# Performance work log

Hardware: AMD Instinct MI355X
Metric: run time of the kernel (lower is better)

Reference implementation:

```python
import jax, jax.numpy as jnp
import numpy as np

N_NODES = 50000
N_EDGES = 600000
IN_FEATS = 128
HIDDEN = 256
OUT_FEATS = 64


def setup_inputs() -> dict:
    key = jax.random.key(0)
    ks = jax.random.split(key, 12)
    inv = lambda n: 1.0 / np.sqrt(n)
    return {
        "x": jax.random.normal(ks[0], (N_NODES, IN_FEATS), dtype=jnp.float32),
        "edge_index": jax.random.randint(ks[1], (2, N_EDGES), 0, N_NODES, dtype=jnp.int64),
        "W_sage": jax.random.normal(ks[2], (IN_FEATS, IN_FEATS), dtype=jnp.float32) * inv(IN_FEATS),
        "W1a": jax.random.normal(ks[3], (IN_FEATS, HIDDEN), dtype=jnp.float32) * inv(IN_FEATS),
        "b1a": jax.random.normal(ks[4], (HIDDEN,), dtype=jnp.float32) * 0.01,
        "W1b": jax.random.normal(ks[5], (HIDDEN, OUT_FEATS), dtype=jnp.float32) * inv(HIDDEN),
        "b1b": jax.random.normal(ks[6], (OUT_FEATS,), dtype=jnp.float32) * 0.01,
        "W2a": jax.random.normal(ks[7], (IN_FEATS, HIDDEN), dtype=jnp.float32) * inv(IN_FEATS),
        "b2a": jax.random.normal(ks[8], (HIDDEN,), dtype=jnp.float32) * 0.01,
        "W2b": jax.random.normal(ks[9], (HIDDEN, OUT_FEATS), dtype=jnp.float32) * inv(HIDDEN),
        "b2b": jax.random.normal(ks[10], (OUT_FEATS,), dtype=jnp.float32) * 0.01,
    }


def reference(x, edge_index, W_sage, W1a, b1a, W1b, b1b, W2a, b2a, W2b, b2b):
    n = x.shape[0]
    src, dst = edge_index[0], edge_index[1]
    # SAGEConv mean aggregation: mean over incoming neighbor (source) features at each target node
    summed = jax.ops.segment_sum(x[src], dst, num_segments=n)          # [N, in]
    deg = jax.ops.segment_sum(jnp.ones_like(src, dtype=x.dtype), dst, num_segments=n)
    mean = summed / jnp.maximum(deg, 1.0)[:, None]                     # nodes w/o neighbors -> 0
    x_1hop = mean @ W_sage                                             # lin_l, no root, no bias
    # dual MLP branches (dropout is identity in eval mode)
    out1 = jax.nn.relu(x @ W1a + b1a) @ W1b + b1b
    out2 = jax.nn.relu(x_1hop @ W2a + b2a) @ W2b + b2b
    return out1 + out2
```

## Files before the change

### kernel.cpp

```cpp
#include <hip/hip_runtime.h>

#define N_NODES 50000
#define N_PAD   50048
#define N_EDGES 600000
#define IN_F 128
#define HID 256
#define OUT_F 64
#define ROWS 16
#define SLOTS 56
#define NBLK (N_PAD / ROWS)

typedef __attribute__((ext_vector_type(8))) short bf16x8;
typedef __attribute__((ext_vector_type(4))) float f32x4;

__device__ inline short f2bf(float f) {
    unsigned u = __builtin_bit_cast(unsigned, f);
    u += 0x7fffu + ((u >> 16) & 1u);
    return (short)(u >> 16);
}
__device__ inline float bflo(unsigned u) { return __builtin_bit_cast(float, u << 16); }
__device__ inline float bfhi(unsigned u) { return __builtin_bit_cast(float, u & 0xffff0000u); }

__global__ __launch_bounds__(256) void k0_kernel(
    const float* __restrict__ Wsg, const float* __restrict__ W2a,
    float* __restrict__ Wc, int* __restrict__ cursor)
{
    const int bid = blockIdx.x, t = threadIdx.x;
    if (bid < 128) {
        float acc = 0.f;
        #pragma unroll 8
        for (int j = 0; j < 128; ++j)
            acc = fmaf(Wsg[bid * 128 + j], W2a[j * 256 + t], acc);
        Wc[bid * 256 + t] = acc;
    } else {
        int i = (bid - 128) * 256 + t;
        if (i < N_PAD) cursor[i] = 0;
    }
}

__global__ __launch_bounds__(256) void prep_build_kernel(
    const float* __restrict__ x, short* __restrict__ xb,
    const float* __restrict__ W1a, const float* __restrict__ W1b,
    const float* __restrict__ Wc,  const float* __restrict__ W2b,
    short* __restrict__ F1a, short* __restrict__ F1b,
    short* __restrict__ Fc,  short* __restrict__ F2b,
    const int* __restrict__ ei, int* __restrict__ cursor,
    unsigned short* __restrict__ esrc)
{
    const int bid = blockIdx.x, t = threadIdx.x;
    if (bid < 3125) {
        int i = bid * 256 + t;
        float4 a0 = *reinterpret_cast<const float4*>(x + (size_t)i * 8);
        float4 a1 = *reinterpret_cast<const float4*>(x + (size_t)i * 8 + 4);
        bf16x8 v;
        v[0] = f2bf(a0.x); v[1] = f2bf(a0.y); v[2] = f2bf(a0.z); v[3] = f2bf(a0.w);
        v[4] = f2bf(a1.x); v[5] = f2bf(a1.y); v[6] = f2bf(a1.z); v[7] = f2bf(a1.w);
        *reinterpret_cast<bf16x8*>(xb + (size_t)i * 8) = v;
    } else if (bid < 3173) {
        int cid = (bid - 3125) * 256 + t;
        const float* src; short* dst; int N, KST, base;
        if      (cid < 4096)  { src = W1a; dst = F1a; N = 256; KST = 4; base = 0; }
        else if (cid < 6144)  { src = W1b; dst = F1b; N = 64;  KST = 8; base = 4096; }
        else if (cid < 10240) { src = Wc;  dst = Fc;  N = 256; KST = 4; base = 6144; }
        else                  { src = W2b; dst = F2b; N = 64;  KST = 8; base = 10240; }
        int c = cid - base;
        int lane = c & 63;
        int rem = c >> 6;
        int ks = rem % KST;
        int nt = rem / KST;
        int col = nt * 16 + (lane & 15);
        int k0 = ks * 32 + (lane >> 4) * 8;
        bf16x8 v;
        #pragma unroll
        for (int j = 0; j < 8; ++j)
            v[j] = f2bf(src[(size_t)(k0 + j) * N + col]);
        *reinterpret_cast<bf16x8*>(dst + (size_t)c * 8) = v;
    } else {
        int e = (bid - 3173) * 256 + t;
        if (e < N_EDGES) {
            int src = ei[e];
            int dst = ei[N_EDGES + e];
            int p = atomicAdd(&cursor[dst], 1);
            if (p < SLOTS) esrc[(size_t)dst * SLOTS + p] = (unsigned short)src;
        }
    }
}

__device__ inline bf16x8 afrag_lds128(const short* S, int lane, int ks) {
    int row = lane & 15, g = lane >> 4;
    int chunk = (ks * 4 + g) ^ row;
    return *reinterpret_cast<const bf16x8*>(
        reinterpret_cast<const char*>(S) + row * 256 + chunk * 16);
}
__device__ inline bf16x8 afrag_lds256(const short* S, int lane, int ks) {
    int row = lane & 15, g = lane >> 4;
    int chunk = (ks * 4 + g) ^ row;
    return *reinterpret_cast<const bf16x8*>(
        reinterpret_cast<const char*>(S) + row * 512 + chunk * 16);
}

__device__ inline void stage1_relu(const bf16x8 afr[4], short* Hs,
                                   const short* __restrict__ Waf,
                                   const float* __restrict__ ba,
                                   int w, int lane)
{
    const int row16 = lane & 15, g = lane >> 4;
    #pragma unroll
    for (int i = 0; i < 4; ++i) {
        int nt = w * 4 + i;
        f32x4 acc = {0.f, 0.f, 0.f, 0.f};
        #pragma unroll
        for (int ks = 0; ks < 4; ++ks) {
            bf16x8 b = *reinterpret_cast<const bf16x8*>(
                Waf + ((size_t)(nt * 4 + ks) * 64 + lane) * 8);
            acc = __builtin_amdgcn_mfma_f32_16x16x32_bf16(afr[ks], b, acc, 0, 0, 0);
        }
        int col = nt * 16 + row16;
        float bias = ba[col];
        #pragma unroll
        for (int reg = 0; reg < 4; ++reg) {
            int hrow = g * 4 + reg;
            float v = fmaxf(acc[reg] + bias, 0.0f);
            *reinterpret_cast<short*>(reinterpret_cast<char*>(Hs)
                + hrow * 512 + ((((col >> 3) ^ hrow) & 31) * 16) + (col & 7) * 2) = f2bf(v);
        }
    }
}

__device__ inline f32x4 stage2_acc(const short* Hs, const short* __restrict__ Wbf,
                                   int w, int lane, f32x4 acc)
{
    #pragma unroll
    for (int ks = 0; ks < 8; ++ks) {
        bf16x8 a = afrag_lds256(Hs, lane, ks);
        bf16x8 b = *reinterpret_cast<const bf16x8*>(
            Wbf + ((size_t)(w * 8 + ks) * 64 + lane) * 8);
        acc = __builtin_amdgcn_mfma_f32_16x16x32_bf16(a, b, acc, 0, 0, 0);
    }
    return acc;
}

__global__ __launch_bounds__(256) void fused_kernel(
    const short* __restrict__ xb, const unsigned short* __restrict__ esrc,
    const int* __restrict__ deg,
    const short* __restrict__ F1a, const float* __restrict__ b1a,
    const short* __restrict__ F1b, const float* __restrict__ b1b,
    const short* __restrict__ Fc,  const float* __restrict__ b2a,
    const short* __restrict__ F2b, const float* __restrict__ b2b,
    float* __restrict__ out)
{
    __shared__ short Ms[16 * 128];
    __shared__ short Hs[16 * 256];
    const int t = threadIdx.x, w = t >> 6, lane = t & 63;
    const long r0 = (long)blockIdx.x * ROWS;
    const int row16 = lane & 15, g = lane >> 4;

    #pragma unroll
    for (int nn = 0; nn < 4; ++nn) {
        int row = w * 4 + nn;
        long node = r0 + row;
        int d = deg[node]; d = min(d, SLOTS);
        int slot = min(lane, SLOTS - 1);
        int my = esrc[(size_t)node * SLOTS + slot];
        float ax = 0.f, ay = 0.f;
        for (int j = 0; j < d; j += 16) {
            unsigned u[16];
            #pragma unroll
            for (int k = 0; k < 16; ++k) {
                int cidx = min(j + k, d - 1);
                int s = __builtin_amdgcn_readlane(my, cidx);
                u[k] = *reinterpret_cast<const unsigned*>(xb + (size_t)s * IN_F + lane * 2);
            }
            #pragma unroll
            for (int k = 0; k < 16; ++k) {
                float wk = (j + k < d) ? 1.0f : 0.0f;
                ax = fmaf(bflo(u[k]), wk, ax);
                ay = fmaf(bfhi(u[k]), wk, ay);
            }
        }
        float inv = (d > 0) ? 1.0f / (float)d : 0.0f;
        ax *= inv; ay *= inv;
        int chunk = (lane >> 2) ^ row;
        unsigned packed = (unsigned)(unsigned short)f2bf(ax)
                        | ((unsigned)(unsigned short)f2bf(ay) << 16);
        *reinterpret_cast<unsigned*>(reinterpret_cast<char*>(Ms)
            + row * 256 + chunk * 16 + (lane & 3) * 4) = packed;
    }
    __syncthreads();

    {
        bf16x8 afr[4];
        #pragma unroll
        for (int ks = 0; ks < 4; ++ks) afr[ks] = afrag_lds128(Ms, lane, ks);
        stage1_relu(afr, Hs, Fc, b2a, w, lane);
    }
    __syncthreads();

    f32x4 oacc = {0.f, 0.f, 0.f, 0.f};
    oacc = stage2_acc(Hs, F2b, w, lane, oacc);
    __syncthreads();

    {
        bf16x8 afr[4];
        const short* xrow = xb + (size_t)(r0 + row16) * IN_F + g * 8;
        #pragma unroll
        for (int ks = 0; ks < 4; ++ks)
            afr[ks] = *reinterpret_cast<const bf16x8*>(xrow + ks * 32);
        stage1_relu(afr, Hs, F1a, b1a, w, lane);
    }
    __syncthreads();

    oacc = stage2_acc(Hs, F1b, w, lane, oacc);
    {
        int col = w * 16 + row16;
        float bias = b1b[col] + b2b[col];
        #pragma unroll
        for (int reg = 0; reg < 4; ++reg) {
            long row = r0 + g * 4 + reg;
            if (row < N_NODES)
                out[row * OUT_F + col] = oacc[reg] + bias;
        }
    }
}

extern "C" void kernel_launch(void* const* d_in, const int* in_sizes, int n_in,
                              void* d_out, int out_size, void* d_ws, size_t ws_size,
                              hipStream_t stream)
{
    const float* x   = (const float*)d_in[0];
    const int*   ei  = (const int*)d_in[1];
    const float* Wsg = (const float*)d_in[2];
    const float* W1a = (const float*)d_in[3];
    const float* b1a = (const float*)d_in[4];
    const float* W1b = (const float*)d_in[5];
    const float* b1b = (const float*)d_in[6];
    const float* W2a = (const float*)d_in[7];
    const float* b2a = (const float*)d_in[8];
    const float* W2b = (const float*)d_in[9];
    const float* b2b = (const float*)d_in[10];
    float* out = (float*)d_out;

    int* cursor = (int*)d_ws;
    unsigned short* esrc = (unsigned short*)(cursor + N_PAD);
    float* Wc  = (float*)(esrc + (size_t)N_PAD * SLOTS);
    short* F1a = (short*)(Wc + 128 * 256);
    short* F1b = F1a + 4096 * 8;
    short* Fc  = F1b + 2048 * 8;
    short* F2b = Fc + 4096 * 8;
    short* xb  = F2b + 2048 * 8;

    k0_kernel<<<324, 256, 0, stream>>>(Wsg, W2a, Wc, cursor);
    prep_build_kernel<<<5517, 256, 0, stream>>>(x, xb, W1a, W1b, Wc, W2b,
                                                F1a, F1b, Fc, F2b,
                                                ei, cursor, esrc);
    fused_kernel<<<NBLK, 256, 0, stream>>>(xb, esrc, cursor,
                                           F1a, b1a, F1b, b1b,
                                           Fc, b2a, F2b, b2b, out);
}
```

Measured before the change: 119.6 us.

## Split edge bucketing into its own kernel and fuse weight combine into prep

Removes the separate k0 kernel. The Wsg·W2a product is now computed directly inside the prep kernel's Fc fragment packing, and the cursor is zeroed with hipMemsetAsync. Edge bucketing moves to a dedicated kernel that handles four edges per thread so the loads and atomics are batched. MFMA loops get s_setprio hints to favor matrix issue. Launch count stays the same; the fused Fc path does redundant FMAs per fragment, and the atomic kernel now runs alone instead of alongside the conversions.

```diff
diff --git a/kernel.cpp b/kernel.cpp
--- a/kernel.cpp
+++ b/kernel.cpp
@@ -9,6 +9,7 @@
 #define ROWS 16
 #define SLOTS 56
 #define NBLK (N_PAD / ROWS)
+#define EPT 4
 
 typedef __attribute__((ext_vector_type(8))) short bf16x8;
 typedef __attribute__((ext_vector_type(4))) float f32x4;
@@ -21,31 +22,37 @@
 __device__ inline float bflo(unsigned u) { return __builtin_bit_cast(float, u << 16); }
 __device__ inline float bfhi(unsigned u) { return __builtin_bit_cast(float, u & 0xffff0000u); }
 
-__global__ __launch_bounds__(256) void k0_kernel(
-    const float* __restrict__ Wsg, const float* __restrict__ W2a,
-    float* __restrict__ Wc, int* __restrict__ cursor)
-{
-    const int bid = blockIdx.x, t = threadIdx.x;
-    if (bid < 128) {
-        float acc = 0.f;
-        #pragma unroll 8
-        for (int j = 0; j < 128; ++j)
-            acc = fmaf(Wsg[bid * 128 + j], W2a[j * 256 + t], acc);
-        Wc[bid * 256 + t] = acc;
-    } else {
-        int i = (bid - 128) * 256 + t;
-        if (i < N_PAD) cursor[i] = 0;
-    }
-}
-
-__global__ __launch_bounds__(256) void prep_build_kernel(
-    const float* __restrict__ x, short* __restrict__ xb,
-    const float* __restrict__ W1a, const float* __restrict__ W1b,
-    const float* __restrict__ Wc,  const float* __restrict__ W2b,
-    short* __restrict__ F1a, short* __restrict__ F1b,
-    short* __restrict__ Fc,  short* __restrict__ F2b,
+__global__ __launch_bounds__(256) void build_kernel(
     const int* __restrict__ ei, int* __restrict__ cursor,
     unsigned short* __restrict__ esrc)
+{
+    int t0 = blockIdx.x * (256 * EPT) + threadIdx.x;
+    int src[EPT], dst[EPT], p[EPT];
+    bool v[EPT];
+    #pragma unroll
+    for (int i = 0; i < EPT; ++i) {
+        int e = t0 + i * 256;
+        v[i] = e < N_EDGES;
+        int ee = v[i] ? e : 0;
+        src[i] = ei[ee];
+        dst[i] = ei[N_EDGES + ee];
+    }
+    #pragma unroll
+    for (int i = 0; i < EPT; ++i)
+        p[i] = v[i] ? atomicAdd(&cursor[dst[i]], 1) : SLOTS;
+    #pragma unroll
+    for (int i = 0; i < EPT; ++i)
+        if (v[i] && p[i] < SLOTS)
+            esrc[(size_t)dst[i] * SLOTS + p[i]] = (unsigned short)src[i];
+}
+
+__global__ __launch_bounds__(256) void prep_kernel(
+    const float* __restrict__ x, short* __restrict__ xb,
+    const float* __restrict__ Wsg, const float* __restrict__ W2a,
+    const float* __restrict__ W1a, const float* __restrict__ W1b,
+    const float* __restrict__ W2b,
+    short* __restrict__ F1a, short* __restrict__ F1b,
+    short* __restrict__ Fc,  short* __restrict__ F2b)
 {
     const int bid = blockIdx.x, t = threadIdx.x;
     if (bid < 3125) {
@@ -56,12 +63,36 @@
         v[0] = f2bf(a0.x); v[1] = f2bf(a0.y); v[2] = f2bf(a0.z); v[3] = f2bf(a0.w);
         v[4] = f2bf(a1.x); v[5] = f2bf(a1.y); v[6] = f2bf(a1.z); v[7] = f2bf(a1.w);
         *reinterpret_cast<bf16x8*>(xb + (size_t)i * 8) = v;
-    } else if (bid < 3173) {
-        int cid = (bid - 3125) * 256 + t;
+        return;
+    }
+    int cid = (bid - 3125) * 256 + t;
+    if (cid >= 6144 && cid < 10240) {
+        int c = cid - 6144;
+        int lane = c & 63, rem = c >> 6;
+        int ks = rem & 3, nt = rem >> 2;
+        int col = nt * 16 + (lane & 15);
+        int k0 = ks * 32 + (lane >> 4) * 8;
+        float acc[8] = {0.f, 0.f, 0.f, 0.f, 0.f, 0.f, 0.f, 0.f};
+        for (int m0 = 0; m0 < 128; m0 += 8) {
+            float wcol[8];
+            #pragma unroll
+            for (int mm = 0; mm < 8; ++mm)
+                wcol[mm] = W2a[(size_t)(m0 + mm) * HID + col];
+            #pragma unroll
+            for (int j = 0; j < 8; ++j) {
+                #pragma unroll
+                for (int mm = 0; mm < 8; ++mm)
+                    acc[j] = fmaf(Wsg[(size_t)(k0 + j) * IN_F + m0 + mm], wcol[mm], acc[j]);
+            }
+        }
+        bf16x8 v;
+        #pragma unroll
+        for (int j = 0; j < 8; ++j) v[j] = f2bf(acc[j]);
+        *reinterpret_cast<bf16x8*>(Fc + (size_t)c * 8) = v;
+    } else {
         const float* src; short* dst; int N, KST, base;
         if      (cid < 4096)  { src = W1a; dst = F1a; N = 256; KST = 4; base = 0; }
         else if (cid < 6144)  { src = W1b; dst = F1b; N = 64;  KST = 8; base = 4096; }
-        else if (cid < 10240) { src = Wc;  dst = Fc;  N = 256; KST = 4; base = 6144; }
         else                  { src = W2b; dst = F2b; N = 64;  KST = 8; base = 10240; }
         int c = cid - base;
         int lane = c & 63;
@@ -75,14 +106,6 @@
         for (int j = 0; j < 8; ++j)
             v[j] = f2bf(src[(size_t)(k0 + j) * N + col]);
         *reinterpret_cast<bf16x8*>(dst + (size_t)c * 8) = v;
-    } else {
-        int e = (bid - 3173) * 256 + t;
-        if (e < N_EDGES) {
-            int src = ei[e];
-            int dst = ei[N_EDGES + e];
-            int p = atomicAdd(&cursor[dst], 1);
-            if (p < SLOTS) esrc[(size_t)dst * SLOTS + p] = (unsigned short)src;
-        }
     }
 }
 
@@ -109,12 +132,14 @@
     for (int i = 0; i < 4; ++i) {
         int nt = w * 4 + i;
         f32x4 acc = {0.f, 0.f, 0.f, 0.f};
+        __builtin_amdgcn_s_setprio(1);
         #pragma unroll
         for (int ks = 0; ks < 4; ++ks) {
             bf16x8 b = *reinterpret_cast<const bf16x8*>(
                 Waf + ((size_t)(nt * 4 + ks) * 64 + lane) * 8);
             acc = __builtin_amdgcn_mfma_f32_16x16x32_bf16(afr[ks], b, acc, 0, 0, 0);
         }
+        __builtin_amdgcn_s_setprio(0);
         int col = nt * 16 + row16;
         float bias = ba[col];
         #pragma unroll
@@ -130,6 +155,7 @@
 __device__ inline f32x4 stage2_acc(const short* Hs, const short* __restrict__ Wbf,
                                    int w, int lane, f32x4 acc)
 {
+    __builtin_amdgcn_s_setprio(1);
     #pragma unroll
     for (int ks = 0; ks < 8; ++ks) {
         bf16x8 a = afrag_lds256(Hs, lane, ks);
@@ -137,6 +163,7 @@
             Wbf + ((size_t)(w * 8 + ks) * 64 + lane) * 8);
         acc = __builtin_amdgcn_mfma_f32_16x16x32_bf16(a, b, acc, 0, 0, 0);
     }
+    __builtin_amdgcn_s_setprio(0);
     return acc;
 }
 
@@ -242,17 +269,17 @@
 
     int* cursor = (int*)d_ws;
     unsigned short* esrc = (unsigned short*)(cursor + N_PAD);
-    float* Wc  = (float*)(esrc + (size_t)N_PAD * SLOTS);
-    short* F1a = (short*)(Wc + 128 * 256);
+    short* F1a = (short*)(esrc + (size_t)N_PAD * SLOTS);
     short* F1b = F1a + 4096 * 8;
     short* Fc  = F1b + 2048 * 8;
     short* F2b = Fc + 4096 * 8;
     short* xb  = F2b + 2048 * 8;
 
-    k0_kernel<<<324, 256, 0, stream>>>(Wsg, W2a, Wc, cursor);
-    prep_build_kernel<<<5517, 256, 0, stream>>>(x, xb, W1a, W1b, Wc, W2b,
-                                                F1a, F1b, Fc, F2b,
-                                                ei, cursor, esrc);
+    hipMemsetAsync(cursor, 0, N_PAD * sizeof(int), stream);
+    build_kernel<<<(N_EDGES + 256 * EPT - 1) / (256 * EPT), 256, 0, stream>>>(
+        ei, cursor, esrc);
+    prep_kernel<<<3173, 256, 0, stream>>>(x, xb, Wsg, W2a, W1a, W1b, W2b,
+                                          F1a, F1b, Fc, F2b);
     fused_kernel<<<NBLK, 256, 0, stream>>>(xb, esrc, cursor,
                                            F1a, b1a, F1b, b1b,
                                            Fc, b2a, F2b, b2b, out);
```

Result: no change. 122.0 us (+2.0%).
